# Kernel tuning notes

Measured on AMD Instinct MI355X. Metric: run time of the kernel, lower is better.

Reference implementation:

```python
import jax, jax.numpy as jnp
import numpy as np
from jax import lax

CONF_THRES = 0.25
IOU_THRES = 0.45
MAX_DET = 300      # detections kept after NMS
TOPK = 1024        # candidates entering NMS (sorted by score)
MAX_WH = 7680.0    # class offset for class-aware NMS
NC = 80            # classes
NM = 32            # mask prototypes
IMG = 640          # network input size
PROTO_HW = 160     # proto map resolution (IMG/4)
EPS = 1e-7


def xywh2xyxy(x):
    cx, cy, w, h = x[:, 0], x[:, 1], x[:, 2], x[:, 3]
    return jnp.stack([cx - w / 2, cy - h / 2, cx + w / 2, cy + h / 2], axis=1)


def box_iou(box1, box2):
    # box1: [K,4], box2: [M,4] in xyxy -> [K,M]
    a1, a2 = box1[:, None, :2], box1[:, None, 2:]
    b1, b2 = box2[None, :, :2], box2[None, :, 2:]
    inter = jnp.clip(jnp.minimum(a2, b2) - jnp.maximum(a1, b1), 0).prod(-1)
    area1 = (a2 - a1).prod(-1)
    area2 = (b2 - b1).prod(-1)
    return inter / (area1 + area2 - inter + EPS)


def greedy_nms_keep(boxes, valid, iou_thres):
    # boxes already sorted by descending score; returns bool keep mask [K]
    K = boxes.shape[0]
    sup = box_iou(boxes, boxes) > iou_thres  # [K,K]
    lower = jnp.arange(K)

    def body(i, keep):
        suppressed = jnp.any(keep & sup[:, i] & (lower < i))
        return keep.at[i].set(valid[i] & ~suppressed)

    return lax.fori_loop(0, K, body, jnp.zeros((K,), dtype=bool))


def setup_inputs() -> dict:
    key = jax.random.key(0)
    k1, k2, k3, k4, k5, k6 = jax.random.split(key, 6)
    N = 25200
    cxcy = jax.random.uniform(k1, (1, N, 2), jnp.float32, 0.0, float(IMG))
    wh = jax.random.uniform(k2, (1, N, 2), jnp.float32, 5.0, 120.0)
    obj = jax.random.uniform(k3, (1, N, 1), jnp.float32)
    cls = jax.random.uniform(k4, (1, N, NC), jnp.float32)
    coef = jax.random.normal(k5, (1, N, NM), jnp.float32) * 0.5
    prediction = jnp.concatenate([cxcy, wh, obj, cls, coef], axis=2)  # [1,N,117]
    protos = jax.random.normal(k6, (NM, PROTO_HW, PROTO_HW), jnp.float32)
    return {"prediction": prediction, "protos": protos}


def reference(prediction, protos):
    x = prediction[0]                       # [N, 5+NC+NM]
    obj = x[:, 4]
    cls_conf = x[:, 5:5 + NC] * obj[:, None]  # x[:,5:] *= x[:,4:5]
    conf = cls_conf.max(axis=1)
    j = jnp.argmax(cls_conf, axis=1)
    valid_all = (obj > CONF_THRES) & (conf > CONF_THRES)

    boxes_all = xywh2xyxy(x[:, :4])
    scores_masked = jnp.where(valid_all, conf, -1.0)
    top_scores, idx = lax.top_k(scores_masked, TOPK)  # sorted descending

    b = boxes_all[idx]              # [TOPK,4], no class offset
    cls_id = j[idx]                 # [TOPK]
    coef = x[idx, 5 + NC:]          # [TOPK,NM]
    valid = top_scores > CONF_THRES

    nms_boxes = b + (cls_id.astype(b.dtype) * MAX_WH)[:, None]  # class-aware
    keep = greedy_nms_keep(nms_boxes, valid, IOU_THRES)

    keep_scores = jnp.where(keep, top_scores, -1.0)
    fs, i2 = lax.top_k(keep_scores, MAX_DET)
    fvalid = fs > CONF_THRES
    fb = b[i2] * fvalid[:, None].astype(b.dtype)
    fcls = jnp.where(fvalid, cls_id[i2], -1)
    fcoef = coef[i2] * fvalid[:, None].astype(coef.dtype)
    fs = jnp.where(fvalid, fs, 0.0)

    # process_mask_native
    m = jax.nn.sigmoid(fcoef @ protos.reshape(NM, -1))          # [MAX_DET, HW*HW]
    m = m.reshape(MAX_DET, PROTO_HW, PROTO_HW)
    m = jax.image.resize(m, (MAX_DET, IMG, IMG), method='bilinear')
    x1, y1, x2, y2 = fb[:, 0], fb[:, 1], fb[:, 2], fb[:, 3]
    r = jnp.arange(IMG, dtype=fb.dtype)[None, None, :]  # along width vs x
    c = jnp.arange(IMG, dtype=fb.dtype)[None, :, None]  # along height vs y
    crop = ((r >= x1[:, None, None]) & (r < x2[:, None, None]) &
            (c >= y1[:, None, None]) & (c < y2[:, None, None]))
    masks_f = m * crop.astype(m.dtype) * fvalid[:, None, None].astype(m.dtype)
    masks_bool = masks_f > 0.5
    return masks_f, masks_bool, fb, fs, fcls
```

## Files before the change

### kernel.cpp

```cpp
#include <hip/hip_runtime.h>

constexpr int   kNA     = 25200;
constexpr int   kStride = 117;
constexpr int   kNC     = 80;
constexpr int   kNM     = 32;
constexpr int   kTopK   = 1024;
constexpr int   kMaxDet = 300;
constexpr int   kImg    = 640;
constexpr int   kPHW    = 160;
constexpr float kConfT  = 0.25f;
constexpr float kIouT   = 0.45f;
constexpr float kMaxWH  = 7680.0f;

constexpr unsigned long long kMaskElems = 300ull * 640ull * 640ull;

typedef float v4f __attribute__((ext_vector_type(4)));

constexpr size_t kN4       = 61440000;
constexpr size_t kQSlices  = 30720000;
constexpr int    kQPerSlice= 102400;
constexpr int    kQPerRow  = 160;

constexpr size_t kZDecE  = 6144000;
constexpr size_t kZTopkE = 15360000;
constexpr size_t kZSupE  = 18432000;
constexpr size_t kZNmsE  = 24576000;

constexpr int kZDecB  = 1024;
constexpr int kZTopkB = 512;
constexpr int kZSupB  = 256;
constexpr int kZNmsB  = 512;
constexpr int kZFinB  = 1280;

constexpr size_t O_SCORES = 0;
constexpr size_t O_BOXES  = 100864;
constexpr size_t O_CLS    = 504064;
constexpr size_t O_TKIDX  = 604864;
constexpr size_t O_TKSC   = 608960;
constexpr size_t O_TKBOX  = 613056;
constexpr size_t O_TKNBOX = 629440;
constexpr size_t O_TKCLS  = 645824;
constexpr size_t O_SUP    = 649984;
constexpr size_t O_NDET   = 782336;
constexpr size_t O_DBOX   = 782400;
constexpr size_t O_DCOEF  = 787264;
constexpr size_t O_ROWR   = 825664;

constexpr int kDecRows = 64;
constexpr int kDecThr  = 128;
constexpr int kDecBlocks = (kNA + kDecRows - 1) / kDecRows;
__global__ __launch_bounds__(kDecThr) void decode_k(const float* __restrict__ pred,
        float* __restrict__ scores, float* __restrict__ boxes, int* __restrict__ cls,
        float* __restrict__ outz) {
    if (blockIdx.x >= kDecBlocks) {
        v4f z = 0.f;
        size_t stride = (size_t)(gridDim.x - kDecBlocks) * kDecThr;
        for (size_t i = (size_t)(blockIdx.x - kDecBlocks) * kDecThr + threadIdx.x;
             i < kZDecE; i += stride)
            __builtin_nontemporal_store(z, ((v4f*)outz) + i);
        return;
    }
    __shared__ float rows[kDecRows * kStride];
    int base = blockIdx.x * kDecRows;
    int nrows = min(kDecRows, kNA - base);
    int total = nrows * kStride;
    const float* src = pred + (size_t)base * kStride;
    for (int i = threadIdx.x; i < total; i += kDecThr) rows[i] = src[i];
    __syncthreads();
    int r = threadIdx.x;
    if (r >= nrows) return;
    int a = base + r;
    const float* p = rows + r * kStride;
    float obj = p[4];
    float best = -1.0f; int bj = 0;
    for (int c = 0; c < kNC; ++c) {
        float v = p[5 + c] * obj;
        if (v > best) { best = v; bj = c; }
    }
    bool valid = (obj > kConfT) && (best > kConfT);
    scores[a] = valid ? best : -1.0f;
    float cx = p[0], cy = p[1], w = p[2], h = p[3];
    float hw = w * 0.5f, hh = h * 0.5f;
    boxes[4*a+0] = cx - hw; boxes[4*a+1] = cy - hh;
    boxes[4*a+2] = cx + hw; boxes[4*a+3] = cy + hh;
    cls[a] = bj;
}

__device__ __forceinline__ unsigned f2ord(float f) {
    unsigned b = __float_as_uint(f);
    return (b & 0x80000000u) ? ~b : (b | 0x80000000u);
}
__device__ __forceinline__ float ord2f(unsigned u) {
    unsigned b = (u & 0x80000000u) ? (u ^ 0x80000000u) : ~u;
    return __uint_as_float(b);
}

__global__ __launch_bounds__(1024) void topk_k(const float* __restrict__ scores,
        const float* __restrict__ boxes, const int* __restrict__ cls,
        int* __restrict__ tk_idx, float* __restrict__ tk_sc, float* __restrict__ tk_box,
        float* __restrict__ tk_nbox, int* __restrict__ tk_cls,
        float* __restrict__ outz) {
    if (blockIdx.x != 0) {
        v4f z = 0.f;
        size_t stride = (size_t)(gridDim.x - 1) * 1024;
        for (size_t i = kZDecE + (size_t)(blockIdx.x - 1) * 1024 + threadIdx.x;
             i < kZTopkE; i += stride)
            __builtin_nontemporal_store(z, ((v4f*)outz) + i);
        return;
    }
    __shared__ unsigned long long keys[kTopK];
    __shared__ int wcnt[16];
    __shared__ unsigned sh_cnt;
    int tid = threadIdx.x;
    int lane = tid & 63, wid = tid >> 6;

    unsigned uv[25];
#pragma unroll
    for (int k = 0; k < 25; ++k) {
        int i = tid + k * 1024;
        uv[k] = (i < kNA) ? f2ord(scores[i]) : 0u;
    }

    unsigned lo = 0u, hi = 0xFFFFFFFFu;
    for (int it = 0; it < 34; ++it) {
        unsigned mid;
        if (it == 0)      mid = 0xBE800000u;
        else if (it == 1) mid = 0xBF800001u;
        else {
            mid = (unsigned)(((unsigned long long)lo + (unsigned long long)hi) >> 1);
            if (mid == lo) break;
        }
        if (mid <= lo || mid >= hi) continue;
        int c = 0;
#pragma unroll
        for (int k = 0; k < 25; ++k) c += (uv[k] >= mid);
#pragma unroll
        for (int off = 32; off >= 1; off >>= 1) c += __shfl_down(c, off);
        __syncthreads();
        if (lane == 0) wcnt[wid] = c;
        __syncthreads();
        int tot = 0;
#pragma unroll
        for (int w = 0; w < 16; ++w) tot += wcnt[w];
        if (tot >= kTopK) lo = mid; else hi = mid;
    }
    unsigned uT = lo;

    int nGreater;
    {
        int c = 0;
#pragma unroll
        for (int k = 0; k < 25; ++k) c += (uv[k] >= uT + 1u);
#pragma unroll
        for (int off = 32; off >= 1; off >>= 1) c += __shfl_down(c, off);
        __syncthreads();
        if (lane == 0) wcnt[wid] = c;
        __syncthreads();
        int t = 0;
#pragma unroll
        for (int w = 0; w < 16; ++w) t += wcnt[w];
        nGreater = t;
    }
    int krem = kTopK - nGreater;
    if (tid == 0) sh_cnt = 0;
    __syncthreads();

#pragma unroll
    for (int k = 0; k < 25; ++k) {
        int i = tid + k * 1024;
        unsigned u = uv[k];
        if (i < kNA && u > uT) {
            unsigned p = atomicAdd(&sh_cnt, 1u);
            keys[p] = ((unsigned long long)u << 32) | (unsigned)(~i);
        }
    }

    int ilo = 0, ihi = kNA;
    while (ilo < ihi) {
        int mid = (ilo + ihi) >> 1;
        int c = 0;
#pragma unroll
        for (int k = 0; k < 25; ++k) {
            int i = tid + k * 1024;
            c += (i < mid && uv[k] == uT);
        }
#pragma unroll
        for (int off = 32; off >= 1; off >>= 1) c += __shfl_down(c, off);
        __syncthreads();
        if (lane == 0) wcnt[wid] = c;
        __syncthreads();
        int cc = 0;
#pragma unroll
        for (int w = 0; w < 16; ++w) cc += wcnt[w];
        if (cc >= krem) ihi = mid; else ilo = mid + 1;
    }
#pragma unroll
    for (int k = 0; k < 25; ++k) {
        int i = tid + k * 1024;
        if (i < ilo && uv[k] == uT) {
            unsigned p = atomicAdd(&sh_cnt, 1u);
            keys[p] = ((unsigned long long)uT << 32) | (unsigned)(~i);
        }
    }
    __syncthreads();

    for (int k2 = 2; k2 <= kTopK; k2 <<= 1) {
        for (int j = k2 >> 1; j > 0; j >>= 1) {
            int partner = tid ^ j;
            unsigned long long a = keys[tid], b = keys[partner];
            bool iLower = (tid & j) == 0;
            bool descRegion = (tid & k2) == 0;
            unsigned long long mx = (a > b) ? a : b;
            unsigned long long mn = (a > b) ? b : a;
            unsigned long long res = (iLower == descRegion) ? mx : mn;
            __syncthreads();
            keys[tid] = res;
            __syncthreads();
        }
    }

    unsigned long long key = keys[tid];
    unsigned u = (unsigned)(key >> 32);
    int idx = (int)(~((unsigned)key));
    tk_idx[tid] = idx;
    tk_sc[tid]  = ord2f(u);
    float4 bx = ((const float4*)boxes)[idx];
    ((float4*)tk_box)[tid] = bx;
    int cid = cls[idx];
    float off = (float)cid * kMaxWH;
    float4 nb; nb.x = bx.x + off; nb.y = bx.y + off; nb.z = bx.z + off; nb.w = bx.w + off;
    ((float4*)tk_nbox)[tid] = nb;
    tk_cls[tid] = cid;
}

__global__ __launch_bounds__(256) void supmat_k(const float* __restrict__ tk_nbox,
                                                unsigned long long* __restrict__ sup,
                                                float* __restrict__ outz) {
    if (blockIdx.x >= 64) {
        v4f z = 0.f;
        size_t stride = (size_t)(gridDim.x - 64) * 256;
        for (size_t i = kZTopkE + (size_t)(blockIdx.x - 64) * 256 + threadIdx.x;
             i < kZSupE; i += stride)
            __builtin_nontemporal_store(z, ((v4f*)outz) + i);
        return;
    }
    __shared__ float4 bxs[kTopK];
    int tid = threadIdx.x;
    for (int k = tid; k < kTopK; k += 256) bxs[k] = ((const float4*)tk_nbox)[k];
    __syncthreads();
    int r = tid >> 4, w = tid & 15;
    int i = blockIdx.x * 16 + r;
    float4 a = bxs[i];
    float areaA = (a.z - a.x) * (a.w - a.y);
    unsigned long long bits = 0;
    for (int l = 0; l < 64; ++l) {
        float4 b = bxs[w * 64 + l];
        float xx1 = fmaxf(a.x, b.x), yy1 = fmaxf(a.y, b.y);
        float xx2 = fminf(a.z, b.z), yy2 = fminf(a.w, b.w);
        float iw = fmaxf(xx2 - xx1, 0.f), ih = fmaxf(yy2 - yy1, 0.f);
        float inter = iw * ih;
        float areaB = (b.z - b.x) * (b.w - b.y);
        float iou = inter / (areaA + areaB - inter + 1e-7f);
        if (iou > kIouT) bits |= 1ull << l;
    }
    sup[(size_t)i * 16 + w] = bits;
}

__global__ __launch_bounds__(256) void nms_k(const float* __restrict__ pred,
        const float* __restrict__ tk_sc, const int* __restrict__ tk_idx,
        const float* __restrict__ tk_box, const int* __restrict__ tk_cls,
        const unsigned long long* __restrict__ sup,
        int* __restrict__ ndet, float* __restrict__ out,
        float* __restrict__ dbox, float* __restrict__ dcoef,
        int2* __restrict__ rowr) {
    if (blockIdx.x != 0) {
        v4f z = 0.f;
        size_t stride = (size_t)(gridDim.x - 1) * 256;
        for (size_t i = kZSupE + (size_t)(blockIdx.x - 1) * 256 + threadIdx.x;
             i < kZNmsE; i += stride)
            __builtin_nontemporal_store(z, ((v4f*)out) + i);
        return;
    }
    __shared__ unsigned long long buf[2][1024];
    __shared__ int dslot_lds[kMaxDet];
    __shared__ int sh_nd;
    int tid = threadIdx.x;
    int lane = tid & 63;

    unsigned long long vW = 0;
    if (tid < 64) {
        for (int b = 0; b < 16; ++b) {
            unsigned long long bw = __ballot(tk_sc[b * 64 + lane] > kConfT);
            if (lane == b) vW = bw;
        }
    }
    for (int i = tid; i < 1024; i += 256) buf[0][i] = sup[i];

    unsigned long long supW = 0;
    unsigned long long kws[16];
    for (int b = 0; b < 16; ++b) {
        __syncthreads();
        if (tid >= 64) {
            if (b + 1 < 16) {
                for (int i = tid - 64; i < 1024; i += 192)
                    buf[(b + 1) & 1][i] = sup[(size_t)(b + 1) * 1024 + i];
            }
        } else {
            const unsigned long long* ch = buf[b & 1];
            unsigned long long s  = __shfl(supW, b);
            unsigned long long vb = __shfl(vW, b);
            unsigned long long kw = 0;
            unsigned long long rbuf[8];
            int w16 = lane & 15;
#pragma unroll
            for (int p = 0; p < 8; ++p) rbuf[p] = ch[p * 16 + w16];
            for (int l = 0; l < 64; ++l) {
                unsigned long long rw = rbuf[l & 7];
                if (l + 8 < 64) rbuf[l & 7] = ch[(l + 8) * 16 + w16];
                unsigned long long rb = __shfl(rw, b);
                bool kp = ((vb >> l) & 1ull) && !((s >> l) & 1ull);
                if (kp) { kw |= 1ull << l; s |= rb; supW |= rw; }
            }
            kws[b] = kw;
        }
    }
    if (tid == 0) {
        int d = 0;
        for (int b = 0; b < 16 && d < kMaxDet; ++b) {
            unsigned long long kw = kws[b];
            for (int l = 0; l < 64 && d < kMaxDet; ++l)
                if ((kw >> l) & 1ull) dslot_lds[d++] = b * 64 + l;
        }
        sh_nd = d;
        *ndet = d;
    }
    __syncthreads();

    int n = sh_nd;
    float* fb   = out + 2 * kMaskElems;
    float* fs   = fb + kMaxDet * 4;
    float* fcls = fs + kMaxDet;
    for (int d = tid; d < kMaxDet; d += 256) {
        int2 rr; rr.x = 1; rr.y = 0;
        if (d < n) {
            int t = dslot_lds[d];
            int a = tk_idx[t];
            float4 bx = ((const float4*)tk_box)[t];
            fb[4*d+0] = bx.x; fb[4*d+1] = bx.y; fb[4*d+2] = bx.z; fb[4*d+3] = bx.w;
            fs[d] = tk_sc[t];
            fcls[d] = (float)tk_cls[t];
            ((float4*)dbox)[d] = bx;
            const float* cp = pred + (size_t)a * kStride + 5 + kNC;
            for (int c = 0; c < kNM; ++c) dcoef[d * kNM + c] = cp[c];
            int i_lo = max(0, (int)ceilf(bx.y));
            int i_hi = min(kImg - 1, (int)ceilf(bx.w) - 1);
            int j_lo = max(0, (int)ceilf(bx.x));
            int j_hi = min(kImg - 1, (int)ceilf(bx.z) - 1);
            if (i_lo <= i_hi && j_lo <= j_hi) { rr.x = i_lo; rr.y = i_hi; }
        } else {
            fb[4*d+0] = 0.f; fb[4*d+1] = 0.f; fb[4*d+2] = 0.f; fb[4*d+3] = 0.f;
            fs[d] = 0.f; fcls[d] = -1.0f;
            float4 z; z.x = z.y = z.z = z.w = 0.f;
            ((float4*)dbox)[d] = z;
            for (int c = 0; c < kNM; ++c) dcoef[d * kNM + c] = 0.f;
        }
        rowr[d] = rr;
    }
}

constexpr int kPatch = 34;

__global__ __launch_bounds__(256) void finalize_k(const float* __restrict__ protos,
        const float* __restrict__ dbox, const float* __restrict__ dcoef,
        const int2* __restrict__ rowr, float* __restrict__ out) {
    int tid = threadIdx.x;
    if (blockIdx.x >= kMaxDet) {
        __shared__ int2 rr_lds[kMaxDet];
        for (int t = tid; t < kMaxDet; t += 256) rr_lds[t] = rowr[t];
        __syncthreads();
        v4f z = 0.f;
        size_t stride = (size_t)(gridDim.x - kMaxDet) * 256;
        for (size_t q = kZNmsE + (size_t)(blockIdx.x - kMaxDet) * 256 + tid;
             q < kN4; q += stride) {
            size_t qr = (q >= kQSlices) ? (q - kQSlices) : q;
            int d = (int)(qr / kQPerSlice);
            int rowq = (int)(qr - (size_t)d * kQPerSlice);
            int i = rowq / kQPerRow;
            int2 rr = rr_lds[d];
            if (i < rr.x || i > rr.y)
                __builtin_nontemporal_store(z, ((v4f*)out) + q);
        }
        return;
    }
    int d = blockIdx.x;
    int2 rr = rowr[d];
    if (rr.x > rr.y) return;
    float4 bx = ((const float4*)dbox)[d];
    float x1 = bx.x, y1 = bx.y, x2 = bx.z, y2 = bx.w;
    int i_lo = rr.x, i_hi = rr.y;
    int j_lo = max(0, (int)ceilf(x1));
    int j_hi = min(kImg - 1, (int)ceilf(x2) - 1);

    int py_lo = min(159, max(0, (int)floorf(((float)i_lo + 0.5f) * 0.25f - 0.5f)));
    int py_hi = min(159, max(0, (int)floorf(((float)i_hi + 0.5f) * 0.25f - 0.5f) + 1));
    int px_lo = min(159, max(0, (int)floorf(((float)j_lo + 0.5f) * 0.25f - 0.5f)));
    int px_hi = min(159, max(0, (int)floorf(((float)j_hi + 0.5f) * 0.25f - 0.5f) + 1));
    int ph = py_hi - py_lo + 1, pw = px_hi - px_lo + 1;
    if (ph > kPatch) ph = kPatch;
    if (pw > kPatch) pw = kPatch;

    __shared__ float coef[kNM];
    __shared__ float patch[kPatch * kPatch];
    if (tid < kNM) coef[tid] = dcoef[d * kNM + tid];
    __syncthreads();
    int cells = ph * pw;
    for (int c = tid; c < cells; c += 256) {
        int py = py_lo + c / pw, px = px_lo + c % pw;
        const float* pp = protos + (size_t)py * kPHW + px;
        float z = 0.f;
#pragma unroll
        for (int m = 0; m < kNM; ++m) z = fmaf(coef[m], pp[(size_t)m * kPHW * kPHW], z);
        patch[c] = 1.0f / (1.0f + expf(-z));
    }
    __syncthreads();

    float* mf = out + (size_t)d * (kImg * kImg);
    float* mb = out + kMaskElems + (size_t)d * (kImg * kImg);
    int H = i_hi - i_lo + 1;
    int work = H * kQPerRow;
    for (int w = tid; w < work; w += 256) {
        int rrow = w / kQPerRow;
        int jq = w - rrow * kQPerRow;
        int i = i_lo + rrow;
        float sy = fminf(fmaxf(((float)i + 0.5f) * 0.25f - 0.5f, 0.f), 159.f);
        int yy0 = (int)sy; float fy = sy - (float)yy0;
        int yy1i = min(yy0 + 1, 159);
        const float* prow0 = &patch[(yy0 - py_lo) * pw - px_lo];
        const float* prow1 = &patch[(yy1i - py_lo) * pw - px_lo];
        v4f vf = 0.f;
        v4f vb = 0.f;
        int j0 = jq * 4;
#pragma unroll
        for (int t = 0; t < 4; ++t) {
            int j = j0 + t;
            if (j >= j_lo && j <= j_hi) {
                float sx = fminf(fmaxf(((float)j + 0.5f) * 0.25f - 0.5f, 0.f), 159.f);
                int xx0 = (int)sx; float fx = sx - (float)xx0;
                int xx1i = min(xx0 + 1, 159);
                float v00 = prow0[xx0], v01 = prow0[xx1i];
                float v10 = prow1[xx0], v11 = prow1[xx1i];
                float top = (1.f - fx) * v00 + fx * v01;
                float bot = (1.f - fx) * v10 + fx * v11;
                float m = (1.f - fy) * top + fy * bot;
                vf[t] = m;
                vb[t] = (m > 0.5f) ? 1.f : 0.f;
            }
        }
        __builtin_nontemporal_store(vf, (v4f*)(mf + (size_t)i * kImg + j0));
        __builtin_nontemporal_store(vb, (v4f*)(mb + (size_t)i * kImg + j0));
    }
}

extern "C" void kernel_launch(void* const* d_in, const int* in_sizes, int n_in,
                              void* d_out, int out_size, void* d_ws, size_t ws_size,
                              hipStream_t stream) {
    const float* pred   = (const float*)d_in[0];
    const float* protos = (const float*)d_in[1];
    float* out = (float*)d_out;
    char* ws = (char*)d_ws;

    float* s_scores = (float*)(ws + O_SCORES);
    float* s_boxes  = (float*)(ws + O_BOXES);
    int*   s_cls    = (int*)  (ws + O_CLS);
    int*   tk_idx   = (int*)  (ws + O_TKIDX);
    float* tk_sc    = (float*)(ws + O_TKSC);
    float* tk_box   = (float*)(ws + O_TKBOX);
    float* tk_nbox  = (float*)(ws + O_TKNBOX);
    int*   tk_cls   = (int*)  (ws + O_TKCLS);
    unsigned long long* sup = (unsigned long long*)(ws + O_SUP);
    int*   ndet     = (int*)  (ws + O_NDET);
    float* dbox     = (float*)(ws + O_DBOX);
    float* dcoef    = (float*)(ws + O_DCOEF);
    int2*  rowr     = (int2*) (ws + O_ROWR);

    decode_k<<<dim3(kDecBlocks + kZDecB), dim3(kDecThr), 0, stream>>>(pred, s_scores, s_boxes, s_cls, out);
    topk_k<<<dim3(1 + kZTopkB), dim3(1024), 0, stream>>>(s_scores, s_boxes, s_cls,
                                               tk_idx, tk_sc, tk_box, tk_nbox, tk_cls, out);
    supmat_k<<<dim3(64 + kZSupB), dim3(256), 0, stream>>>(tk_nbox, sup, out);
    nms_k<<<dim3(1 + kZNmsB), dim3(256), 0, stream>>>(pred, tk_sc, tk_idx, tk_box, tk_cls, sup,
                                             ndet, out, dbox, dcoef, rowr);
    finalize_k<<<dim3(kMaxDet + kZFinB), dim3(256), 0, stream>>>(protos, dbox, dcoef, rowr, out);
}
```

Before: 1.169 ms.

## Restrict mask writes to box column span and rebalance zero-fill across kernels

```diff
diff --git a/kernel.cpp b/kernel.cpp
--- a/kernel.cpp
+++ b/kernel.cpp
@@ -16,21 +16,21 @@
 
 typedef float v4f __attribute__((ext_vector_type(4)));
 
-constexpr size_t kN4       = 61440000;
-constexpr size_t kQSlices  = 30720000;
-constexpr int    kQPerSlice= 102400;
-constexpr int    kQPerRow  = 160;
-
-constexpr size_t kZDecE  = 6144000;
-constexpr size_t kZTopkE = 15360000;
-constexpr size_t kZSupE  = 18432000;
-constexpr size_t kZNmsE  = 24576000;
+constexpr size_t   kN4        = 61440000;
+constexpr size_t   kQSlices   = 30720000;
+constexpr unsigned kQPerSlice = 102400;
+constexpr unsigned kQPerRow   = 160;
+
+constexpr size_t kZ0 = 5000000;
+constexpr size_t kZ1 = 14500000;
+constexpr size_t kZ2 = 18000000;
+constexpr size_t kZ3 = 24000000;
 
 constexpr int kZDecB  = 1024;
 constexpr int kZTopkB = 512;
-constexpr int kZSupB  = 256;
-constexpr int kZNmsB  = 512;
-constexpr int kZFinB  = 1280;
+constexpr int kZSupB  = 384;
+constexpr int kZNmsB  = 768;
+constexpr int kZFinB  = 2048;
 
 constexpr size_t O_SCORES = 0;
 constexpr size_t O_BOXES  = 100864;
@@ -56,7 +56,7 @@
         v4f z = 0.f;
         size_t stride = (size_t)(gridDim.x - kDecBlocks) * kDecThr;
         for (size_t i = (size_t)(blockIdx.x - kDecBlocks) * kDecThr + threadIdx.x;
-             i < kZDecE; i += stride)
+             i < kZ0; i += stride)
             __builtin_nontemporal_store(z, ((v4f*)outz) + i);
         return;
     }
@@ -103,8 +103,8 @@
     if (blockIdx.x != 0) {
         v4f z = 0.f;
         size_t stride = (size_t)(gridDim.x - 1) * 1024;
-        for (size_t i = kZDecE + (size_t)(blockIdx.x - 1) * 1024 + threadIdx.x;
-             i < kZTopkE; i += stride)
+        for (size_t i = kZ0 + (size_t)(blockIdx.x - 1) * 1024 + threadIdx.x;
+             i < kZ1; i += stride)
             __builtin_nontemporal_store(z, ((v4f*)outz) + i);
         return;
     }
@@ -239,8 +239,8 @@
     if (blockIdx.x >= 64) {
         v4f z = 0.f;
         size_t stride = (size_t)(gridDim.x - 64) * 256;
-        for (size_t i = kZTopkE + (size_t)(blockIdx.x - 64) * 256 + threadIdx.x;
-             i < kZSupE; i += stride)
+        for (size_t i = kZ1 + (size_t)(blockIdx.x - 64) * 256 + threadIdx.x;
+             i < kZ2; i += stride)
             __builtin_nontemporal_store(z, ((v4f*)outz) + i);
         return;
     }
@@ -272,12 +272,12 @@
         const unsigned long long* __restrict__ sup,
         int* __restrict__ ndet, float* __restrict__ out,
         float* __restrict__ dbox, float* __restrict__ dcoef,
-        int2* __restrict__ rowr) {
+        int4* __restrict__ rowr) {
     if (blockIdx.x != 0) {
         v4f z = 0.f;
         size_t stride = (size_t)(gridDim.x - 1) * 256;
-        for (size_t i = kZSupE + (size_t)(blockIdx.x - 1) * 256 + threadIdx.x;
-             i < kZNmsE; i += stride)
+        for (size_t i = kZ2 + (size_t)(blockIdx.x - 1) * 256 + threadIdx.x;
+             i < kZ3; i += stride)
             __builtin_nontemporal_store(z, ((v4f*)out) + i);
         return;
     }
@@ -341,7 +341,7 @@
     float* fs   = fb + kMaxDet * 4;
     float* fcls = fs + kMaxDet;
     for (int d = tid; d < kMaxDet; d += 256) {
-        int2 rr; rr.x = 1; rr.y = 0;
+        int4 rr; rr.x = 1; rr.y = 0; rr.z = 1; rr.w = 0;
         if (d < n) {
             int t = dslot_lds[d];
             int a = tk_idx[t];
@@ -356,7 +356,9 @@
             int i_hi = min(kImg - 1, (int)ceilf(bx.w) - 1);
             int j_lo = max(0, (int)ceilf(bx.x));
             int j_hi = min(kImg - 1, (int)ceilf(bx.z) - 1);
-            if (i_lo <= i_hi && j_lo <= j_hi) { rr.x = i_lo; rr.y = i_hi; }
+            if (i_lo <= i_hi && j_lo <= j_hi) {
+                rr.x = i_lo; rr.y = i_hi; rr.z = j_lo >> 2; rr.w = j_hi >> 2;
+            }
         } else {
             fb[4*d+0] = 0.f; fb[4*d+1] = 0.f; fb[4*d+2] = 0.f; fb[4*d+3] = 0.f;
             fs[d] = 0.f; fcls[d] = -1.0f;
@@ -372,34 +374,36 @@
 
 __global__ __launch_bounds__(256) void finalize_k(const float* __restrict__ protos,
         const float* __restrict__ dbox, const float* __restrict__ dcoef,
-        const int2* __restrict__ rowr, float* __restrict__ out) {
+        const int4* __restrict__ rowr, float* __restrict__ out) {
     int tid = threadIdx.x;
     if (blockIdx.x >= kMaxDet) {
-        __shared__ int2 rr_lds[kMaxDet];
+        __shared__ int4 rr_lds[kMaxDet];
         for (int t = tid; t < kMaxDet; t += 256) rr_lds[t] = rowr[t];
         __syncthreads();
         v4f z = 0.f;
         size_t stride = (size_t)(gridDim.x - kMaxDet) * 256;
-        for (size_t q = kZNmsE + (size_t)(blockIdx.x - kMaxDet) * 256 + tid;
+        for (size_t q = kZ3 + (size_t)(blockIdx.x - kMaxDet) * 256 + tid;
              q < kN4; q += stride) {
-            size_t qr = (q >= kQSlices) ? (q - kQSlices) : q;
-            int d = (int)(qr / kQPerSlice);
-            int rowq = (int)(qr - (size_t)d * kQPerSlice);
-            int i = rowq / kQPerRow;
-            int2 rr = rr_lds[d];
-            if (i < rr.x || i > rr.y)
+            unsigned qr = (unsigned)((q >= kQSlices) ? (q - kQSlices) : q);
+            unsigned d    = qr / kQPerSlice;
+            unsigned rowq = qr - d * kQPerSlice;
+            unsigned i    = rowq / kQPerRow;
+            unsigned jq   = rowq - i * kQPerRow;
+            int4 rr = rr_lds[d];
+            bool own = ((int)i >= rr.x) & ((int)i <= rr.y) &
+                       ((int)jq >= rr.z) & ((int)jq <= rr.w);
+            if (!own)
                 __builtin_nontemporal_store(z, ((v4f*)out) + q);
         }
         return;
     }
     int d = blockIdx.x;
-    int2 rr = rowr[d];
+    int4 rr = rowr[d];
     if (rr.x > rr.y) return;
     float4 bx = ((const float4*)dbox)[d];
-    float x1 = bx.x, y1 = bx.y, x2 = bx.z, y2 = bx.w;
     int i_lo = rr.x, i_hi = rr.y;
-    int j_lo = max(0, (int)ceilf(x1));
-    int j_hi = min(kImg - 1, (int)ceilf(x2) - 1);
+    int j_lo = max(0, (int)ceilf(bx.x));
+    int j_hi = min(kImg - 1, (int)ceilf(bx.z) - 1);
 
     int py_lo = min(159, max(0, (int)floorf(((float)i_lo + 0.5f) * 0.25f - 0.5f)));
     int py_hi = min(159, max(0, (int)floorf(((float)i_hi + 0.5f) * 0.25f - 0.5f) + 1));
@@ -426,12 +430,14 @@
 
     float* mf = out + (size_t)d * (kImg * kImg);
     float* mb = out + kMaskElems + (size_t)d * (kImg * kImg);
-    int H = i_hi - i_lo + 1;
-    int work = H * kQPerRow;
+    int H  = i_hi - i_lo + 1;
+    int nq = rr.w - rr.z + 1;
+    int work = H * nq;
     for (int w = tid; w < work; w += 256) {
-        int rrow = w / kQPerRow;
-        int jq = w - rrow * kQPerRow;
-        int i = i_lo + rrow;
+        int rrow = w / nq;
+        int jqo  = w - rrow * nq;
+        int i  = i_lo + rrow;
+        int j0 = (rr.z + jqo) * 4;
         float sy = fminf(fmaxf(((float)i + 0.5f) * 0.25f - 0.5f, 0.f), 159.f);
         int yy0 = (int)sy; float fy = sy - (float)yy0;
         int yy1i = min(yy0 + 1, 159);
@@ -439,7 +445,6 @@
         const float* prow1 = &patch[(yy1i - py_lo) * pw - px_lo];
         v4f vf = 0.f;
         v4f vb = 0.f;
-        int j0 = jq * 4;
 #pragma unroll
         for (int t = 0; t < 4; ++t) {
             int j = j0 + t;
@@ -481,7 +486,7 @@
     int*   ndet     = (int*)  (ws + O_NDET);
     float* dbox     = (float*)(ws + O_DBOX);
     float* dcoef    = (float*)(ws + O_DCOEF);
-    int2*  rowr     = (int2*) (ws + O_ROWR);
+    int4*  rowr     = (int4*) (ws + O_ROWR);
 
     decode_k<<<dim3(kDecBlocks + kZDecB), dim3(kDecThr), 0, stream>>>(pred, s_scores, s_boxes, s_cls, out);
     topk_k<<<dim3(1 + kZTopkB), dim3(1024), 0, stream>>>(s_scores, s_boxes, s_cls,
```

Result: no change. 1.170 ms (+0.1%).
